# Kernel tuning notes

Hardware: AMD Instinct MI355X
Metric: run time of the kernel (lower is better)

Reference implementation:

```python
import jax, jax.numpy as jnp
import numpy as np

N = 50000      # nodes
E = 800000     # edges (before self-loops)
F_IN = 128     # nfeat
H = 4          # heads
C = 64         # GAT out_channels per head
HID = 128      # GCN hidden
NCLASS = 10
NEG = 0.2      # leaky-relu negative slope (alpha)


def setup_inputs() -> dict:
    key = jax.random.key(0)
    ks = jax.random.split(key, 10)
    init = lambda k, shape, fan: jax.random.normal(k, shape, jnp.float32) / np.sqrt(fan).astype(np.float32)
    return {
        "x": jax.random.normal(ks[0], (N, F_IN), jnp.float32),
        "edge_attr": jax.random.normal(ks[1], (E, 8), jnp.float32),  # ignored (edge_dim=None in GATConv)
        "Wg": init(ks[2], (F_IN, H * C), F_IN),
        "att_src": init(ks[3], (H, C), C),
        "att_dst": init(ks[4], (H, C), C),
        "bg": jnp.zeros((H * C,), jnp.float32),
        "Wc": init(ks[5], (H * C, HID), H * C),
        "bc": jnp.zeros((HID,), jnp.float32),
        "Wl": init(ks[6], (HID, NCLASS), HID),
        "bl": jnp.zeros((NCLASS,), jnp.float32),
        "edge_index": jax.random.randint(ks[7], (2, E), 0, N, dtype=jnp.int64),
    }


def reference(x, edge_attr, Wg, att_src, att_dst, bg, Wc, bc, Wl, bl, edge_index):
    del edge_attr  # GATConv with edge_dim=None ignores edge_attr
    loop = jnp.arange(N, dtype=edge_index.dtype)
    src = jnp.concatenate([edge_index[0], loop])  # message sources j (add_self_loops=True)
    dst = jnp.concatenate([edge_index[1], loop])  # message targets i

    # ---- GATConv (concat=True) ----
    h = (x @ Wg).reshape(N, H, C)                     # [N,H,C]
    a_s = jnp.einsum('nhc,hc->nh', h, att_src)        # [N,H]
    a_d = jnp.einsum('nhc,hc->nh', h, att_dst)
    e = a_s[src] + a_d[dst]                           # [E2,H]
    e = jnp.where(e > 0, e, NEG * e)                  # leaky_relu
    m = jax.ops.segment_max(e, dst, num_segments=N)   # segment softmax over incoming edges
    ex = jnp.exp(e - m[dst])
    denom = jax.ops.segment_sum(ex, dst, num_segments=N)
    alpha = ex / denom[dst]                           # [E2,H]
    agg = jax.ops.segment_sum(alpha[:, :, None] * h[src], dst, num_segments=N)  # [N,H,C]
    xg = jax.nn.elu(agg.reshape(N, H * C) + bg)

    # ---- GCNConv (sym-normalized SpMM with self-loops) ----
    deg = jax.ops.segment_sum(jnp.ones_like(dst, dtype=jnp.float32), dst, num_segments=N)
    dinv = jnp.where(deg > 0, 1.0 / jnp.sqrt(deg), 0.0)
    norm = dinv[src] * dinv[dst]                      # [E2]
    xw = xg @ Wc                                      # [N,HID]
    xc = jax.ops.segment_sum(norm[:, None] * xw[src], dst, num_segments=N) + bc
    xc = jax.nn.relu(xc)

    # ---- classifier head ----
    logits = xc @ Wl + bl                             # [N,NCLASS]
    return jax.nn.log_softmax(logits, axis=1)
```

## Files before the change

### kernel.cpp

```cpp
#include <hip/hip_runtime.h>
#include <hip/hip_fp16.h>
#include <math.h>

#define NN 50000
#define EE 800000
#define E2 (EE + NN)
#define FIN 128
#define HC 256
#define HID 128
#define NCLS 10
#define NEG 0.2f
#define NB2 196
#define NBLK 256
#define WPART ((E2 + NBLK - 1) / NBLK)

typedef _Float16 f16x8 __attribute__((ext_vector_type(8)));
typedef float f32x4 __attribute__((ext_vector_type(4)));

#define FMA_MIX_LO(acc, u, w) \
    asm("v_fma_mix_f32 %0, %1, %2, %0 op_sel:[0,0,0] op_sel_hi:[1,0,0]" \
        : "+v"(acc) : "v"(u), "v"(w))
#define FMA_MIX_HI(acc, u, w) \
    asm("v_fma_mix_f32 %0, %1, %2, %0 op_sel:[1,0,0] op_sel_hi:[1,0,0]" \
        : "+v"(acc) : "v"(u), "v"(w))

__device__ inline uint pack2h(float a, float b) {
    return (uint)__half_as_ushort(__float2half(a)) |
           ((uint)__half_as_ushort(__float2half(b)) << 16);
}

__global__ __launch_bounds__(256) void prep_kernel(const float* __restrict__ Wg,
                                                   const float* __restrict__ Wc,
                                                   const float* __restrict__ att_s,
                                                   const float* __restrict__ att_d,
                                                   ushort* __restrict__ wgt,
                                                   ushort* __restrict__ wct,
                                                   float4* __restrict__ vs,
                                                   float4* __restrict__ vd) {
    int i = blockIdx.x * 256 + threadIdx.x;
    if (i < HC * FIN) {
        int c = i & 255, k = i >> 8;
        wgt[c * FIN + k] = __half_as_ushort(__float2half(Wg[i]));
        int c2 = i & 127, k2 = i >> 7;
        wct[c2 * HC + k2] = __half_as_ushort(__float2half(Wc[i]));
    }
    if (blockIdx.x == 0 && threadIdx.x < FIN) {
        int k = threadIdx.x;
        float s[4] = {0.f, 0.f, 0.f, 0.f}, d[4] = {0.f, 0.f, 0.f, 0.f};
        for (int h = 0; h < 4; ++h)
            for (int c = 0; c < 64; ++c) {
                float wv = Wg[k * HC + h * 64 + c];
                s[h] += wv * att_s[h * 64 + c];
                d[h] += wv * att_d[h * 64 + c];
            }
        vs[k] = make_float4(s[0], s[1], s[2], s[3]);
        vd[k] = make_float4(d[0], d[1], d[2], d[3]);
    }
}

__global__ __launch_bounds__(256) void prep_x(const float* __restrict__ x,
                                              const float4* __restrict__ vs,
                                              const float4* __restrict__ vd,
                                              ushort* __restrict__ x_half,
                                              float* __restrict__ a_s,
                                              float* __restrict__ a_d) {
    const int node = blockIdx.x * 4 + (threadIdx.x >> 6);
    const int lane = threadIdx.x & 63;
    if (node >= NN) return;
    float2 xv = ((const float2*)(x + (size_t)node * FIN))[lane];
    ((uint*)x_half)[(size_t)node * 64 + lane] = pack2h(xv.x, xv.y);
    float4 v0 = vs[2 * lane], v1 = vs[2 * lane + 1];
    float4 d0 = vd[2 * lane], d1 = vd[2 * lane + 1];
    float ps0 = xv.x * v0.x + xv.y * v1.x;
    float ps1 = xv.x * v0.y + xv.y * v1.y;
    float ps2 = xv.x * v0.z + xv.y * v1.z;
    float ps3 = xv.x * v0.w + xv.y * v1.w;
    float pd0 = xv.x * d0.x + xv.y * d1.x;
    float pd1 = xv.x * d0.y + xv.y * d1.y;
    float pd2 = xv.x * d0.z + xv.y * d1.z;
    float pd3 = xv.x * d0.w + xv.y * d1.w;
#pragma unroll
    for (int m = 32; m >= 1; m >>= 1) {
        ps0 += __shfl_xor(ps0, m, 64); ps1 += __shfl_xor(ps1, m, 64);
        ps2 += __shfl_xor(ps2, m, 64); ps3 += __shfl_xor(ps3, m, 64);
        pd0 += __shfl_xor(pd0, m, 64); pd1 += __shfl_xor(pd1, m, 64);
        pd2 += __shfl_xor(pd2, m, 64); pd3 += __shfl_xor(pd3, m, 64);
    }
    if (lane == 0) {
        ((float4*)a_s)[node] = make_float4(ps0, ps1, ps2, ps3);
        ((float4*)a_d)[node] = make_float4(pd0, pd1, pd2, pd3);
    }
}

__global__ __launch_bounds__(256) void hist_coarse(const int* __restrict__ ei,
                                                   uint* __restrict__ blockhist) {
    __shared__ uint h[NB2];
    for (int i = threadIdx.x; i < NB2; i += 256) h[i] = 0;
    __syncthreads();
    int e0 = blockIdx.x * WPART, e1 = min(E2, e0 + WPART);
    for (int e = e0 + threadIdx.x; e < e1; e += 256) {
        int dst = (e < EE) ? ei[EE + e] : e - EE;
        atomicAdd(&h[dst >> 8], 1u);
    }
    __syncthreads();
    for (int i = threadIdx.x; i < NB2; i += 256) blockhist[i * NBLK + blockIdx.x] = h[i];
}

__global__ __launch_bounds__(256) void scan_blocks(const uint* __restrict__ blockhist,
                                                   uint* __restrict__ blockoff,
                                                   uint* __restrict__ total) {
    __shared__ uint sh[256];
    int b = blockIdx.x, t = threadIdx.x;
    uint v = blockhist[b * NBLK + t];
    sh[t] = v;
    __syncthreads();
#pragma unroll
    for (int off = 1; off < 256; off <<= 1) {
        uint y = (t >= off) ? sh[t - off] : 0;
        __syncthreads();
        sh[t] += y;
        __syncthreads();
    }
    blockoff[b * NBLK + t] = sh[t] - v;
    if (t == 255) total[b] = sh[255];
}

__global__ __launch_bounds__(256) void reorder_kernel(const int* __restrict__ ei,
                                                      const uint* __restrict__ blockoff,
                                                      const uint* __restrict__ total,
                                                      uint* __restrict__ ebuf) {
    __shared__ uint sh[256];
    __shared__ uint cur[NB2];
    int t = threadIdx.x;
    uint v = (t < NB2) ? total[t] : 0;
    sh[t] = v;
    __syncthreads();
#pragma unroll
    for (int off = 1; off < 256; off <<= 1) {
        uint y = (t >= off) ? sh[t - off] : 0;
        __syncthreads();
        sh[t] += y;
        __syncthreads();
    }
    if (t < NB2) cur[t] = (sh[t] - v) + blockoff[t * NBLK + blockIdx.x];
    __syncthreads();
    int e0 = blockIdx.x * WPART, e1 = min(E2, e0 + WPART);
    for (int e = e0 + t; e < e1; e += 256) {
        int src, dst;
        if (e < EE) { src = ei[e]; dst = ei[EE + e]; }
        else        { src = dst = e - EE; }
        uint p = atomicAdd(&cur[dst >> 8], 1u);
        ebuf[p] = (uint)src | ((uint)(dst & 255) << 16);
    }
}

__global__ __launch_bounds__(256) void bucket_csr(const uint* __restrict__ ebuf,
                                                  const uint* __restrict__ total,
                                                  int* __restrict__ row_start,
                                                  float* __restrict__ dinv,
                                                  ushort* __restrict__ csr_src) {
    __shared__ uint ldeg[256], lcur[256], sh[256];
    __shared__ uint sbe[2];
    const int b = blockIdx.x, t = threadIdx.x;
    uint v = (t < NB2) ? total[t] : 0;
    sh[t] = v;
    __syncthreads();
#pragma unroll
    for (int off = 1; off < 256; off <<= 1) {
        uint y = (t >= off) ? sh[t - off] : 0;
        __syncthreads();
        sh[t] += y;
        __syncthreads();
    }
    if (t == b) { sbe[0] = sh[t] - v; sbe[1] = sh[t]; }
    ldeg[t] = 0;
    __syncthreads();
    const uint base = sbe[0], end = sbe[1];
    for (uint i = base + t; i < end; i += 256) atomicAdd(&ldeg[ebuf[i] >> 16], 1u);
    __syncthreads();
    uint dv = ldeg[t];
    sh[t] = dv;
    __syncthreads();
#pragma unroll
    for (int off = 1; off < 256; off <<= 1) {
        uint y = (t >= off) ? sh[t - off] : 0;
        __syncthreads();
        sh[t] += y;
        __syncthreads();
    }
    uint lscan = sh[t] - dv;
    int node = b * 256 + t;
    if (node < NN) {
        row_start[node] = (int)(base + lscan);
        dinv[node] = rsqrtf((float)dv);
    }
    lcur[t] = base + lscan;
    __syncthreads();
    for (uint i = base + t; i < end; i += 256) {
        uint pk = ebuf[i];
        uint p = atomicAdd(&lcur[pk >> 16], 1u);
        csr_src[p] = (ushort)(pk & 0xFFFFu);
    }
    if (b == 0 && t == 0) row_start[NN] = E2;
}

__global__ __launch_bounds__(256) void gat_fused(const ushort* __restrict__ x_half,
                                                 const float* __restrict__ a_s,
                                                 const float* __restrict__ a_d,
                                                 const int* __restrict__ row_start,
                                                 const ushort* __restrict__ csr_src,
                                                 const ushort* __restrict__ wgt,
                                                 const float* __restrict__ bg,
                                                 const ushort* __restrict__ wct,
                                                 ushort* __restrict__ xw) {
    __shared__ ushort yt[16][520];
    __shared__ ushort xt[16][264];
    __shared__ ushort xt2[16][136];
    __shared__ int    lds_off[4][64];
    __shared__ float4 lds_ex[4][64];

    const int t = threadIdx.x;
    const int w = t >> 6;
    const int lane = t & 63;
    const int lr = lane & 15;
    const int lg = lane >> 4;
    const int rowbase = blockIdx.x * 16;

    const char* xbase = (const char*)x_half;
    const uint lane4 = (uint)lane * 4;

    for (int i = 0; i < 4; ++i) {
        const int nl = 4 * w + i;
        const int node = rowbase + nl;
        const int s0 = row_start[node], s1 = row_start[node + 1];
        const float4 ad = ((const float4*)a_d)[node];

        float den0 = 0.f, den1 = 0.f, den2 = 0.f, den3 = 0.f;
        float a00=0.f,a01=0.f,a10=0.f,a11=0.f,a20=0.f,a21=0.f,a30=0.f,a31=0.f;

#define GAT_BODY(J)                                                \
    {                                                              \
        int off = lds_off[w][J];                                   \
        float4 ex = lds_ex[w][J];                                  \
        uint u = *(const uint*)(xbase + ((uint)off + lane4));      \
        FMA_MIX_LO(a00, u, ex.x); FMA_MIX_HI(a01, u, ex.x);        \
        FMA_MIX_LO(a10, u, ex.y); FMA_MIX_HI(a11, u, ex.y);        \
        FMA_MIX_LO(a20, u, ex.z); FMA_MIX_HI(a21, u, ex.z);        \
        FMA_MIX_LO(a30, u, ex.w); FMA_MIX_HI(a31, u, ex.w);        \
    }
        for (int e = s0; e < s1; e += 64) {
            const int m = min(64, s1 - e);
            if (lane < m) {
                int src = (int)csr_src[e + lane];
                float4 as = ((const float4*)a_s)[src];
                float v0 = as.x + ad.x; v0 = v0 > 0.f ? v0 : NEG * v0;
                float v1 = as.y + ad.y; v1 = v1 > 0.f ? v1 : NEG * v1;
                float v2 = as.z + ad.z; v2 = v2 > 0.f ? v2 : NEG * v2;
                float v3 = as.w + ad.w; v3 = v3 > 0.f ? v3 : NEG * v3;
                float e0 = __expf(v0); den0 += e0;
                float e1 = __expf(v1); den1 += e1;
                float e2 = __expf(v2); den2 += e2;
                float e3 = __expf(v3); den3 += e3;
                lds_off[w][lane] = src * 256;
                lds_ex[w][lane]  = make_float4(e0, e1, e2, e3);
            }
            asm volatile("s_waitcnt lgkmcnt(0)" ::: "memory");
            int j = 0;
            for (; j + 8 <= m; j += 8) {
                GAT_BODY(j);     GAT_BODY(j + 1); GAT_BODY(j + 2); GAT_BODY(j + 3);
                GAT_BODY(j + 4); GAT_BODY(j + 5); GAT_BODY(j + 6); GAT_BODY(j + 7);
            }
            for (; j < m; ++j) GAT_BODY(j);
            asm volatile("" ::: "memory");
        }
#undef GAT_BODY
#pragma unroll
        for (int m = 32; m >= 1; m >>= 1) {
            den0 += __shfl_xor(den0, m, 64);
            den1 += __shfl_xor(den1, m, 64);
            den2 += __shfl_xor(den2, m, 64);
            den3 += __shfl_xor(den3, m, 64);
        }
        float r0 = 1.f / den0, r1 = 1.f / den1, r2 = 1.f / den2, r3 = 1.f / den3;
        uint* yu = (uint*)&yt[nl][0];
        yu[0 * 64 + lane] = pack2h(a00 * r0, a01 * r0);
        yu[1 * 64 + lane] = pack2h(a10 * r1, a11 * r1);
        yu[2 * 64 + lane] = pack2h(a20 * r2, a21 * r2);
        yu[3 * 64 + lane] = pack2h(a30 * r3, a31 * r3);
    }
    __syncthreads();

    {
        f16x8 bf[4][4];
#pragma unroll
        for (int ct = 0; ct < 4; ++ct)
#pragma unroll
            for (int ks = 0; ks < 4; ++ks)
                bf[ct][ks] = *(const f16x8*)(wgt + (size_t)(64 * w + 16 * ct + lr) * FIN + ks * 32 + 8 * lg);
        float bgv[4];
#pragma unroll
        for (int ct = 0; ct < 4; ++ct) bgv[ct] = bg[64 * w + 16 * ct + lr];

        f32x4 acc[4];
#pragma unroll
        for (int ct = 0; ct < 4; ++ct) acc[ct] = (f32x4){0.f, 0.f, 0.f, 0.f};
#pragma unroll
        for (int ks = 0; ks < 4; ++ks) {
            f16x8 af = *(const f16x8*)&yt[lr][w * 128 + ks * 32 + 8 * lg];
#pragma unroll
            for (int ct = 0; ct < 4; ++ct)
                acc[ct] = __builtin_amdgcn_mfma_f32_16x16x32_f16(af, bf[ct][ks], acc[ct], 0, 0, 0);
        }
#pragma unroll
        for (int j = 0; j < 4; ++j) {
#pragma unroll
            for (int ct = 0; ct < 4; ++ct) {
                float o = acc[ct][j] + bgv[ct];
                o = o > 0.f ? o : __expf(o) - 1.f;
                xt[4 * lg + j][64 * w + 16 * ct + lr] = __half_as_ushort(__float2half(o));
            }
        }
    }
    __syncthreads();

    {
        f16x8 bf2[2][8];
#pragma unroll
        for (int ct = 0; ct < 2; ++ct)
#pragma unroll
            for (int ks = 0; ks < 8; ++ks)
                bf2[ct][ks] = *(const f16x8*)(wct + (size_t)(32 * w + 16 * ct + lr) * HC + ks * 32 + 8 * lg);

        f32x4 acc2[2];
        acc2[0] = (f32x4){0.f, 0.f, 0.f, 0.f};
        acc2[1] = (f32x4){0.f, 0.f, 0.f, 0.f};
#pragma unroll
        for (int ks = 0; ks < 8; ++ks) {
            f16x8 af = *(const f16x8*)&xt[lr][ks * 32 + 8 * lg];
            acc2[0] = __builtin_amdgcn_mfma_f32_16x16x32_f16(af, bf2[0][ks], acc2[0], 0, 0, 0);
            acc2[1] = __builtin_amdgcn_mfma_f32_16x16x32_f16(af, bf2[1][ks], acc2[1], 0, 0, 0);
        }
#pragma unroll
        for (int j = 0; j < 4; ++j) {
#pragma unroll
            for (int ct = 0; ct < 2; ++ct)
                xt2[4 * lg + j][32 * w + 16 * ct + lr] = __half_as_ushort(__float2half(acc2[ct][j]));
        }
    }
    __syncthreads();

    {
        const int rr = t >> 4;
        const int rc = (t & 15) * 8;
        *(uint4*)(xw + (size_t)(rowbase + rr) * HID + rc) = *(const uint4*)&xt2[rr][rc];
    }
}

__global__ __launch_bounds__(256) void gcn_head(const ushort* __restrict__ xw_half,
                                                const int* __restrict__ row_start,
                                                const ushort* __restrict__ csr_src,
                                                const float* __restrict__ dinv,
                                                const float* __restrict__ bc,
                                                const float* __restrict__ Wl,
                                                const float* __restrict__ bl,
                                                float* __restrict__ out) {
    __shared__ int2 lds_ow[4][64];
    const int wid  = threadIdx.x >> 6;
    const int lane = threadIdx.x & 63;
    const int node = blockIdx.x * 4 + wid;
    if (node >= NN) return;
    const int s0 = row_start[node], s1 = row_start[node + 1];
    const float di = dinv[node];
    float ax = 0.f, ay = 0.f;
    const char* xwbase = (const char*)xw_half;
    const uint lane4 = (uint)lane * 4;

#define GCN_BODY(OW)                                            \
    {                                                           \
        uint v = *(const uint*)(xwbase + ((uint)(OW).x + lane4)); \
        float ww = __int_as_float((OW).y);                      \
        FMA_MIX_LO(ax, v, ww); FMA_MIX_HI(ay, v, ww);           \
    }

    for (int e = s0; e < s1; e += 64) {
        const int m = min(64, s1 - e);
        if (lane < m) {
            int s = (int)csr_src[e + lane];
            lds_ow[wid][lane] = make_int2(s * 256, __float_as_int(dinv[s] * di));
        }
        asm volatile("s_waitcnt lgkmcnt(0)" ::: "memory");
        int j = 0;
        for (; j + 8 <= m; j += 8) {
            int2 ow0 = lds_ow[wid][j];
            int2 ow1 = lds_ow[wid][j + 1];
            int2 ow2 = lds_ow[wid][j + 2];
            int2 ow3 = lds_ow[wid][j + 3];
            int2 ow4 = lds_ow[wid][j + 4];
            int2 ow5 = lds_ow[wid][j + 5];
            int2 ow6 = lds_ow[wid][j + 6];
            int2 ow7 = lds_ow[wid][j + 7];
            GCN_BODY(ow0); GCN_BODY(ow1); GCN_BODY(ow2); GCN_BODY(ow3);
            GCN_BODY(ow4); GCN_BODY(ow5); GCN_BODY(ow6); GCN_BODY(ow7);
        }
        for (; j + 4 <= m; j += 4) {
            int2 ow0 = lds_ow[wid][j];
            int2 ow1 = lds_ow[wid][j + 1];
            int2 ow2 = lds_ow[wid][j + 2];
            int2 ow3 = lds_ow[wid][j + 3];
            GCN_BODY(ow0); GCN_BODY(ow1); GCN_BODY(ow2); GCN_BODY(ow3);
        }
        for (; j < m; ++j) {
            int2 ow = lds_ow[wid][j];
            GCN_BODY(ow);
        }
        asm volatile("" ::: "memory");
    }
#undef GCN_BODY
    float2 b = ((const float2*)bc)[lane];
    float o0 = ax + b.x; o0 = o0 > 0.f ? o0 : 0.f;
    float o1 = ay + b.y; o1 = o1 > 0.f ? o1 : 0.f;

    float p[NCLS];
#pragma unroll
    for (int j = 0; j < NCLS; ++j)
        p[j] = o0 * Wl[(2 * lane) * NCLS + j] + o1 * Wl[(2 * lane + 1) * NCLS + j];
#pragma unroll
    for (int m = 32; m >= 1; m >>= 1) {
#pragma unroll
        for (int j = 0; j < NCLS; ++j) p[j] += __shfl_xor(p[j], m, 64);
    }
#pragma unroll
    for (int j = 0; j < NCLS; ++j) p[j] += bl[j];
    float mx = p[0];
#pragma unroll
    for (int j = 1; j < NCLS; ++j) mx = fmaxf(mx, p[j]);
    float s = 0.f;
#pragma unroll
    for (int j = 0; j < NCLS; ++j) s += __expf(p[j] - mx);
    float ls = __logf(s);
    if (lane == 0) {
#pragma unroll
        for (int j = 0; j < NCLS; ++j) out[(size_t)node * NCLS + j] = p[j] - mx - ls;
    }
}

extern "C" void kernel_launch(void* const* d_in, const int* in_sizes, int n_in,
                              void* d_out, int out_size, void* d_ws, size_t ws_size,
                              hipStream_t stream) {
    const float* x       = (const float*)d_in[0];
    const float* Wg      = (const float*)d_in[2];
    const float* att_src = (const float*)d_in[3];
    const float* att_dst = (const float*)d_in[4];
    const float* bg      = (const float*)d_in[5];
    const float* Wc      = (const float*)d_in[6];
    const float* bc      = (const float*)d_in[7];
    const float* Wl      = (const float*)d_in[8];
    const float* bl      = (const float*)d_in[9];
    const int*   ei      = (const int*)d_in[10];
    float* out = (float*)d_out;

    char* p = (char*)d_ws;
    auto alloc = [&](size_t bytes) -> void* {
        void* r = (void*)p;
        p += (bytes + 255) & ~(size_t)255;
        return r;
    };
    ushort* x_half    = (ushort*)alloc((size_t)NN * FIN * 2);
    ushort* xw_half   = (ushort*)alloc((size_t)NN * HID * 2);
    float*  a_s       = (float*)alloc((size_t)NN * 4 * 4);
    float*  a_d       = (float*)alloc((size_t)NN * 4 * 4);
    float*  dinv      = (float*)alloc((size_t)NN * 4);
    int*    row_start = (int*)alloc((size_t)(NN + 1) * 4);
    ushort* csr_src   = (ushort*)alloc((size_t)E2 * 2);
    uint*   ebuf      = (uint*)alloc((size_t)E2 * 4);
    uint*   blockhist = (uint*)alloc((size_t)NB2 * NBLK * 4);
    uint*   blockoff  = (uint*)alloc((size_t)NB2 * NBLK * 4);
    uint*   total     = (uint*)alloc(256 * 4);
    ushort* wgt       = (ushort*)alloc((size_t)HC * FIN * 2);
    ushort* wct       = (ushort*)alloc((size_t)HID * HC * 2);
    float4* vs        = (float4*)alloc(FIN * 16);
    float4* vd        = (float4*)alloc(FIN * 16);

    prep_kernel<<<128, 256, 0, stream>>>(Wg, Wc, att_src, att_dst, wgt, wct, vs, vd);
    prep_x<<<(NN + 3) / 4, 256, 0, stream>>>(x, vs, vd, x_half, a_s, a_d);

    hist_coarse<<<NBLK, 256, 0, stream>>>(ei, blockhist);
    scan_blocks<<<NB2, 256, 0, stream>>>(blockhist, blockoff, total);
    reorder_kernel<<<NBLK, 256, 0, stream>>>(ei, blockoff, total, ebuf);
    bucket_csr<<<NB2, 256, 0, stream>>>(ebuf, total, row_start, dinv, csr_src);

    gat_fused<<<NN / 16, 256, 0, stream>>>(x_half, a_s, a_d, row_start, csr_src,
                                           wgt, bg, wct, xw_half);
    gcn_head<<<(NN + 3) / 4, 256, 0, stream>>>(xw_half, row_start, csr_src, dinv, bc, Wl, bl, out);
}
```

Baseline: 217.1 us.

## Split fused GAT kernel into aggregation and persistent projection GEMM kernels

```diff
diff --git a/kernel.cpp b/kernel.cpp
--- a/kernel.cpp
+++ b/kernel.cpp
@@ -204,109 +204,118 @@
     if (b == 0 && t == 0) row_start[NN] = E2;
 }
 
-__global__ __launch_bounds__(256) void gat_fused(const ushort* __restrict__ x_half,
-                                                 const float* __restrict__ a_s,
-                                                 const float* __restrict__ a_d,
-                                                 const int* __restrict__ row_start,
-                                                 const ushort* __restrict__ csr_src,
-                                                 const ushort* __restrict__ wgt,
-                                                 const float* __restrict__ bg,
-                                                 const ushort* __restrict__ wct,
-                                                 ushort* __restrict__ xw) {
-    __shared__ ushort yt[16][520];
-    __shared__ ushort xt[16][264];
-    __shared__ ushort xt2[16][136];
+__global__ __launch_bounds__(256) void gat_x(const ushort* __restrict__ x_half,
+                                             const float* __restrict__ a_s,
+                                             const float* __restrict__ a_d,
+                                             const int* __restrict__ row_start,
+                                             const ushort* __restrict__ csr_src,
+                                             ushort* __restrict__ y) {
     __shared__ int    lds_off[4][64];
     __shared__ float4 lds_ex[4][64];
-
-    const int t = threadIdx.x;
-    const int w = t >> 6;
-    const int lane = t & 63;
-    const int lr = lane & 15;
-    const int lg = lane >> 4;
-    const int rowbase = blockIdx.x * 16;
-
+    const int wid  = threadIdx.x >> 6;
+    const int lane = threadIdx.x & 63;
+    const int node = blockIdx.x * 4 + wid;
+    if (node >= NN) return;
+    const int s0 = row_start[node], s1 = row_start[node + 1];
+    const float4 ad = ((const float4*)a_d)[node];
+
+    float den0 = 0.f, den1 = 0.f, den2 = 0.f, den3 = 0.f;
+    float a00=0.f,a01=0.f,a10=0.f,a11=0.f,a20=0.f,a21=0.f,a30=0.f,a31=0.f;
     const char* xbase = (const char*)x_half;
     const uint lane4 = (uint)lane * 4;
 
-    for (int i = 0; i < 4; ++i) {
-        const int nl = 4 * w + i;
-        const int node = rowbase + nl;
-        const int s0 = row_start[node], s1 = row_start[node + 1];
-        const float4 ad = ((const float4*)a_d)[node];
-
-        float den0 = 0.f, den1 = 0.f, den2 = 0.f, den3 = 0.f;
-        float a00=0.f,a01=0.f,a10=0.f,a11=0.f,a20=0.f,a21=0.f,a30=0.f,a31=0.f;
-
 #define GAT_BODY(J)                                                \
     {                                                              \
-        int off = lds_off[w][J];                                   \
-        float4 ex = lds_ex[w][J];                                  \
+        int off = lds_off[wid][J];                                 \
+        float4 ex = lds_ex[wid][J];                                \
         uint u = *(const uint*)(xbase + ((uint)off + lane4));      \
         FMA_MIX_LO(a00, u, ex.x); FMA_MIX_HI(a01, u, ex.x);        \
         FMA_MIX_LO(a10, u, ex.y); FMA_MIX_HI(a11, u, ex.y);        \
         FMA_MIX_LO(a20, u, ex.z); FMA_MIX_HI(a21, u, ex.z);        \
         FMA_MIX_LO(a30, u, ex.w); FMA_MIX_HI(a31, u, ex.w);        \
     }
-        for (int e = s0; e < s1; e += 64) {
-            const int m = min(64, s1 - e);
-            if (lane < m) {
-                int src = (int)csr_src[e + lane];
-                float4 as = ((const float4*)a_s)[src];
-                float v0 = as.x + ad.x; v0 = v0 > 0.f ? v0 : NEG * v0;
-                float v1 = as.y + ad.y; v1 = v1 > 0.f ? v1 : NEG * v1;
-                float v2 = as.z + ad.z; v2 = v2 > 0.f ? v2 : NEG * v2;
-                float v3 = as.w + ad.w; v3 = v3 > 0.f ? v3 : NEG * v3;
-                float e0 = __expf(v0); den0 += e0;
-                float e1 = __expf(v1); den1 += e1;
-                float e2 = __expf(v2); den2 += e2;
-                float e3 = __expf(v3); den3 += e3;
-                lds_off[w][lane] = src * 256;
-                lds_ex[w][lane]  = make_float4(e0, e1, e2, e3);
-            }
-            asm volatile("s_waitcnt lgkmcnt(0)" ::: "memory");
-            int j = 0;
-            for (; j + 8 <= m; j += 8) {
-                GAT_BODY(j);     GAT_BODY(j + 1); GAT_BODY(j + 2); GAT_BODY(j + 3);
-                GAT_BODY(j + 4); GAT_BODY(j + 5); GAT_BODY(j + 6); GAT_BODY(j + 7);
-            }
-            for (; j < m; ++j) GAT_BODY(j);
-            asm volatile("" ::: "memory");
-        }
+
+    for (int e = s0; e < s1; e += 64) {
+        const int m = min(64, s1 - e);
+        if (lane < m) {
+            int src = (int)csr_src[e + lane];
+            float4 as = ((const float4*)a_s)[src];
+            float v0 = as.x + ad.x; v0 = v0 > 0.f ? v0 : NEG * v0;
+            float v1 = as.y + ad.y; v1 = v1 > 0.f ? v1 : NEG * v1;
+            float v2 = as.z + ad.z; v2 = v2 > 0.f ? v2 : NEG * v2;
+            float v3 = as.w + ad.w; v3 = v3 > 0.f ? v3 : NEG * v3;
+            float e0 = __expf(v0); den0 += e0;
+            float e1 = __expf(v1); den1 += e1;
+            float e2 = __expf(v2); den2 += e2;
+            float e3 = __expf(v3); den3 += e3;
+            lds_off[wid][lane] = src * 256;
+            lds_ex[wid][lane]  = make_float4(e0, e1, e2, e3);
+        }
+        asm volatile("s_waitcnt lgkmcnt(0)" ::: "memory");
+        int j = 0;
+        for (; j + 8 <= m; j += 8) {
+            GAT_BODY(j);     GAT_BODY(j + 1); GAT_BODY(j + 2); GAT_BODY(j + 3);
+            GAT_BODY(j + 4); GAT_BODY(j + 5); GAT_BODY(j + 6); GAT_BODY(j + 7);
+        }
+        for (; j < m; ++j) GAT_BODY(j);
+        asm volatile("" ::: "memory");
+    }
 #undef GAT_BODY
 #pragma unroll
-        for (int m = 32; m >= 1; m >>= 1) {
-            den0 += __shfl_xor(den0, m, 64);
-            den1 += __shfl_xor(den1, m, 64);
-            den2 += __shfl_xor(den2, m, 64);
-            den3 += __shfl_xor(den3, m, 64);
-        }
-        float r0 = 1.f / den0, r1 = 1.f / den1, r2 = 1.f / den2, r3 = 1.f / den3;
-        uint* yu = (uint*)&yt[nl][0];
-        yu[0 * 64 + lane] = pack2h(a00 * r0, a01 * r0);
-        yu[1 * 64 + lane] = pack2h(a10 * r1, a11 * r1);
-        yu[2 * 64 + lane] = pack2h(a20 * r2, a21 * r2);
-        yu[3 * 64 + lane] = pack2h(a30 * r3, a31 * r3);
-    }
-    __syncthreads();
-
-    {
-        f16x8 bf[4][4];
-#pragma unroll
-        for (int ct = 0; ct < 4; ++ct)
-#pragma unroll
-            for (int ks = 0; ks < 4; ++ks)
-                bf[ct][ks] = *(const f16x8*)(wgt + (size_t)(64 * w + 16 * ct + lr) * FIN + ks * 32 + 8 * lg);
-        float bgv[4];
-#pragma unroll
-        for (int ct = 0; ct < 4; ++ct) bgv[ct] = bg[64 * w + 16 * ct + lr];
-
+    for (int m = 32; m >= 1; m >>= 1) {
+        den0 += __shfl_xor(den0, m, 64);
+        den1 += __shfl_xor(den1, m, 64);
+        den2 += __shfl_xor(den2, m, 64);
+        den3 += __shfl_xor(den3, m, 64);
+    }
+    float r0 = 1.f / den0, r1 = 1.f / den1, r2 = 1.f / den2, r3 = 1.f / den3;
+    uint* yrow = (uint*)y + (size_t)node * 256;
+    yrow[0 * 64 + lane] = pack2h(a00 * r0, a01 * r0);
+    yrow[1 * 64 + lane] = pack2h(a10 * r1, a11 * r1);
+    yrow[2 * 64 + lane] = pack2h(a20 * r2, a21 * r2);
+    yrow[3 * 64 + lane] = pack2h(a30 * r3, a31 * r3);
+}
+
+__global__ __launch_bounds__(256) void proj_gemm2(const ushort* __restrict__ y,
+                                                  const ushort* __restrict__ wgt,
+                                                  const float* __restrict__ bg,
+                                                  const ushort* __restrict__ wct,
+                                                  ushort* __restrict__ xw) {
+    __shared__ ushort xt[16][264];
+    __shared__ ushort xt2[16][136];
+    const int t = threadIdx.x;
+    const int w  = t >> 6;
+    const int l  = t & 63;
+    const int lr = l & 15;
+    const int lg = l >> 4;
+    const int rr = t >> 4;
+    const int rc = (t & 15) * 8;
+
+    f16x8 bf[4][4];
+#pragma unroll
+    for (int ct = 0; ct < 4; ++ct)
+#pragma unroll
+        for (int ks = 0; ks < 4; ++ks)
+            bf[ct][ks] = *(const f16x8*)(wgt + (size_t)(64 * w + 16 * ct + lr) * FIN + ks * 32 + 8 * lg);
+    float bgv[4];
+#pragma unroll
+    for (int ct = 0; ct < 4; ++ct) bgv[ct] = bg[64 * w + 16 * ct + lr];
+
+    f16x8 bf2[2][8];
+#pragma unroll
+    for (int ct = 0; ct < 2; ++ct)
+#pragma unroll
+        for (int ks = 0; ks < 8; ++ks)
+            bf2[ct][ks] = *(const f16x8*)(wct + (size_t)(32 * w + 16 * ct + lr) * HC + ks * 32 + 8 * lg);
+
+    for (int rt = blockIdx.x; rt < 3125; rt += gridDim.x) {
+        const int r0 = rt * 16;
         f32x4 acc[4];
 #pragma unroll
         for (int ct = 0; ct < 4; ++ct) acc[ct] = (f32x4){0.f, 0.f, 0.f, 0.f};
 #pragma unroll
         for (int ks = 0; ks < 4; ++ks) {
-            f16x8 af = *(const f16x8*)&yt[lr][w * 128 + ks * 32 + 8 * lg];
+            f16x8 af = *(const f16x8*)(y + (size_t)(r0 + lr) * 512 + w * 128 + ks * 32 + 8 * lg);
 #pragma unroll
             for (int ct = 0; ct < 4; ++ct)
                 acc[ct] = __builtin_amdgcn_mfma_f32_16x16x32_f16(af, bf[ct][ks], acc[ct], 0, 0, 0);
@@ -320,17 +329,7 @@
                 xt[4 * lg + j][64 * w + 16 * ct + lr] = __half_as_ushort(__float2half(o));
             }
         }
-    }
-    __syncthreads();
-
-    {
-        f16x8 bf2[2][8];
-#pragma unroll
-        for (int ct = 0; ct < 2; ++ct)
-#pragma unroll
-            for (int ks = 0; ks < 8; ++ks)
-                bf2[ct][ks] = *(const f16x8*)(wct + (size_t)(32 * w + 16 * ct + lr) * HC + ks * 32 + 8 * lg);
-
+        __syncthreads();
         f32x4 acc2[2];
         acc2[0] = (f32x4){0.f, 0.f, 0.f, 0.f};
         acc2[1] = (f32x4){0.f, 0.f, 0.f, 0.f};
@@ -346,13 +345,9 @@
             for (int ct = 0; ct < 2; ++ct)
                 xt2[4 * lg + j][32 * w + 16 * ct + lr] = __half_as_ushort(__float2half(acc2[ct][j]));
         }
-    }
-    __syncthreads();
-
-    {
-        const int rr = t >> 4;
-        const int rc = (t & 15) * 8;
-        *(uint4*)(xw + (size_t)(rowbase + rr) * HID + rc) = *(const uint4*)&xt2[rr][rc];
+        __syncthreads();
+        *(uint4*)(xw + (size_t)(r0 + rr) * HID + rc) = *(const uint4*)&xt2[rr][rc];
+        __syncthreads();
     }
 }
 
@@ -466,6 +461,7 @@
         return r;
     };
     ushort* x_half    = (ushort*)alloc((size_t)NN * FIN * 2);
+    ushort* y         = (ushort*)alloc((size_t)NN * 512 * 2);
     ushort* xw_half   = (ushort*)alloc((size_t)NN * HID * 2);
     float*  a_s       = (float*)alloc((size_t)NN * 4 * 4);
     float*  a_d       = (float*)alloc((size_t)NN * 4 * 4);
@@ -489,7 +485,7 @@
     reorder_kernel<<<NBLK, 256, 0, stream>>>(ei, blockoff, total, ebuf);
     bucket_csr<<<NB2, 256, 0, stream>>>(ebuf, total, row_start, dinv, csr_src);
 
-    gat_fused<<<NN / 16, 256, 0, stream>>>(x_half, a_s, a_d, row_start, csr_src,
-                                           wgt, bg, wct, xw_half);
+    gat_x<<<(NN + 3) / 4, 256, 0, stream>>>(x_half, a_s, a_d, row_start, csr_src, y);
+    proj_gemm2<<<1250, 256, 0, stream>>>(y, wgt, bg, wct, xw_half);
     gcn_head<<<(NN + 3) / 4, 256, 0, stream>>>(xw_half, row_start, csr_src, dinv, bc, Wl, bl, out);
 }
```

Measured after the change: 190.9 us. 12.0% less time.

## Process four nodes per block in fused GAT kernel instead of sixteen

Applied to the files above, without the earlier changes.

```diff
diff --git a/kernel.cpp b/kernel.cpp
--- a/kernel.cpp
+++ b/kernel.cpp
@@ -204,44 +204,41 @@
     if (b == 0 && t == 0) row_start[NN] = E2;
 }
 
-__global__ __launch_bounds__(256) void gat_fused(const ushort* __restrict__ x_half,
-                                                 const float* __restrict__ a_s,
-                                                 const float* __restrict__ a_d,
-                                                 const int* __restrict__ row_start,
-                                                 const ushort* __restrict__ csr_src,
-                                                 const ushort* __restrict__ wgt,
-                                                 const float* __restrict__ bg,
-                                                 const ushort* __restrict__ wct,
-                                                 ushort* __restrict__ xw) {
-    __shared__ ushort yt[16][520];
-    __shared__ ushort xt[16][264];
-    __shared__ ushort xt2[16][136];
+__global__ __launch_bounds__(256) void gat_fused2(const ushort* __restrict__ x_half,
+                                                  const float* __restrict__ a_s,
+                                                  const float* __restrict__ a_d,
+                                                  const int* __restrict__ row_start,
+                                                  const ushort* __restrict__ csr_src,
+                                                  const ushort* __restrict__ wgt,
+                                                  const float* __restrict__ bg,
+                                                  const ushort* __restrict__ wct,
+                                                  ushort* __restrict__ xw) {
+    __shared__ ushort yt[4][520];
+    __shared__ ushort xt[4][264];
+    __shared__ ushort xt2[4][136];
     __shared__ int    lds_off[4][64];
     __shared__ float4 lds_ex[4][64];
 
     const int t = threadIdx.x;
-    const int w = t >> 6;
+    const int wid  = t >> 6;
     const int lane = t & 63;
     const int lr = lane & 15;
     const int lg = lane >> 4;
-    const int rowbase = blockIdx.x * 16;
-
-    const char* xbase = (const char*)x_half;
-    const uint lane4 = (uint)lane * 4;
-
-    for (int i = 0; i < 4; ++i) {
-        const int nl = 4 * w + i;
-        const int node = rowbase + nl;
+    const int rowbase = blockIdx.x * 4;
+    const int node = rowbase + wid;
+
+    {
         const int s0 = row_start[node], s1 = row_start[node + 1];
         const float4 ad = ((const float4*)a_d)[node];
-
         float den0 = 0.f, den1 = 0.f, den2 = 0.f, den3 = 0.f;
         float a00=0.f,a01=0.f,a10=0.f,a11=0.f,a20=0.f,a21=0.f,a30=0.f,a31=0.f;
+        const char* xbase = (const char*)x_half;
+        const uint lane4 = (uint)lane * 4;
 
 #define GAT_BODY(J)                                                \
     {                                                              \
-        int off = lds_off[w][J];                                   \
-        float4 ex = lds_ex[w][J];                                  \
+        int off = lds_off[wid][J];                                 \
+        float4 ex = lds_ex[wid][J];                                \
         uint u = *(const uint*)(xbase + ((uint)off + lane4));      \
         FMA_MIX_LO(a00, u, ex.x); FMA_MIX_HI(a01, u, ex.x);        \
         FMA_MIX_LO(a10, u, ex.y); FMA_MIX_HI(a11, u, ex.y);        \
@@ -261,8 +258,8 @@
                 float e1 = __expf(v1); den1 += e1;
                 float e2 = __expf(v2); den2 += e2;
                 float e3 = __expf(v3); den3 += e3;
-                lds_off[w][lane] = src * 256;
-                lds_ex[w][lane]  = make_float4(e0, e1, e2, e3);
+                lds_off[wid][lane] = src * 256;
+                lds_ex[wid][lane]  = make_float4(e0, e1, e2, e3);
             }
             asm volatile("s_waitcnt lgkmcnt(0)" ::: "memory");
             int j = 0;
@@ -282,7 +279,7 @@
             den3 += __shfl_xor(den3, m, 64);
         }
         float r0 = 1.f / den0, r1 = 1.f / den1, r2 = 1.f / den2, r3 = 1.f / den3;
-        uint* yu = (uint*)&yt[nl][0];
+        uint* yu = (uint*)&yt[wid][0];
         yu[0 * 64 + lane] = pack2h(a00 * r0, a01 * r0);
         yu[1 * 64 + lane] = pack2h(a10 * r1, a11 * r1);
         yu[2 * 64 + lane] = pack2h(a20 * r2, a21 * r2);
@@ -296,28 +293,30 @@
         for (int ct = 0; ct < 4; ++ct)
 #pragma unroll
             for (int ks = 0; ks < 4; ++ks)
-                bf[ct][ks] = *(const f16x8*)(wgt + (size_t)(64 * w + 16 * ct + lr) * FIN + ks * 32 + 8 * lg);
+                bf[ct][ks] = *(const f16x8*)(wgt + (size_t)(64 * wid + 16 * ct + lr) * FIN + ks * 32 + 8 * lg);
         float bgv[4];
 #pragma unroll
-        for (int ct = 0; ct < 4; ++ct) bgv[ct] = bg[64 * w + 16 * ct + lr];
+        for (int ct = 0; ct < 4; ++ct) bgv[ct] = bg[64 * wid + 16 * ct + lr];
 
         f32x4 acc[4];
 #pragma unroll
         for (int ct = 0; ct < 4; ++ct) acc[ct] = (f32x4){0.f, 0.f, 0.f, 0.f};
 #pragma unroll
         for (int ks = 0; ks < 4; ++ks) {
-            f16x8 af = *(const f16x8*)&yt[lr][w * 128 + ks * 32 + 8 * lg];
+            f16x8 af = *(const f16x8*)&yt[lr & 3][wid * 128 + ks * 32 + 8 * lg];
 #pragma unroll
             for (int ct = 0; ct < 4; ++ct)
                 acc[ct] = __builtin_amdgcn_mfma_f32_16x16x32_f16(af, bf[ct][ks], acc[ct], 0, 0, 0);
         }
-#pragma unroll
-        for (int j = 0; j < 4; ++j) {
-#pragma unroll
-            for (int ct = 0; ct < 4; ++ct) {
-                float o = acc[ct][j] + bgv[ct];
-                o = o > 0.f ? o : __expf(o) - 1.f;
-                xt[4 * lg + j][64 * w + 16 * ct + lr] = __half_as_ushort(__float2half(o));
+        if (lg == 0) {
+#pragma unroll
+            for (int j = 0; j < 4; ++j) {
+#pragma unroll
+                for (int ct = 0; ct < 4; ++ct) {
+                    float o = acc[ct][j] + bgv[ct];
+                    o = o > 0.f ? o : __expf(o) - 1.f;
+                    xt[j][64 * wid + 16 * ct + lr] = __half_as_ushort(__float2half(o));
+                }
             }
         }
     }
@@ -329,27 +328,29 @@
         for (int ct = 0; ct < 2; ++ct)
 #pragma unroll
             for (int ks = 0; ks < 8; ++ks)
-                bf2[ct][ks] = *(const f16x8*)(wct + (size_t)(32 * w + 16 * ct + lr) * HC + ks * 32 + 8 * lg);
+                bf2[ct][ks] = *(const f16x8*)(wct + (size_t)(32 * wid + 16 * ct + lr) * HC + ks * 32 + 8 * lg);
 
         f32x4 acc2[2];
         acc2[0] = (f32x4){0.f, 0.f, 0.f, 0.f};
         acc2[1] = (f32x4){0.f, 0.f, 0.f, 0.f};
 #pragma unroll
         for (int ks = 0; ks < 8; ++ks) {
-            f16x8 af = *(const f16x8*)&xt[lr][ks * 32 + 8 * lg];
+            f16x8 af = *(const f16x8*)&xt[lr & 3][ks * 32 + 8 * lg];
             acc2[0] = __builtin_amdgcn_mfma_f32_16x16x32_f16(af, bf2[0][ks], acc2[0], 0, 0, 0);
             acc2[1] = __builtin_amdgcn_mfma_f32_16x16x32_f16(af, bf2[1][ks], acc2[1], 0, 0, 0);
         }
-#pragma unroll
-        for (int j = 0; j < 4; ++j) {
-#pragma unroll
-            for (int ct = 0; ct < 2; ++ct)
-                xt2[4 * lg + j][32 * w + 16 * ct + lr] = __half_as_ushort(__float2half(acc2[ct][j]));
-        }
-    }
-    __syncthreads();
-
-    {
+        if (lg == 0) {
+#pragma unroll
+            for (int j = 0; j < 4; ++j) {
+#pragma unroll
+                for (int ct = 0; ct < 2; ++ct)
+                    xt2[j][32 * wid + 16 * ct + lr] = __half_as_ushort(__float2half(acc2[ct][j]));
+            }
+        }
+    }
+    __syncthreads();
+
+    if (t < 64) {
         const int rr = t >> 4;
         const int rc = (t & 15) * 8;
         *(uint4*)(xw + (size_t)(rowbase + rr) * HID + rc) = *(const uint4*)&xt2[rr][rc];
@@ -489,7 +490,7 @@
     reorder_kernel<<<NBLK, 256, 0, stream>>>(ei, blockoff, total, ebuf);
     bucket_csr<<<NB2, 256, 0, stream>>>(ebuf, total, row_start, dinv, csr_src);
 
-    gat_fused<<<NN / 16, 256, 0, stream>>>(x_half, a_s, a_d, row_start, csr_src,
+    gat_fused2<<<NN / 4, 256, 0, stream>>>(x_half, a_s, a_d, row_start, csr_src,
                                            wgt, bg, wct, xw_half);
     gcn_head<<<(NN + 3) / 4, 256, 0, stream>>>(xw_half, row_start, csr_src, dinv, bc, Wl, bl, out);
 }
```

After: 321.3 us. +48.0%, slower.
